# Kernel optimization log

Measured on AMD Instinct MI355X. Metric: run time of the kernel, lower is better.

Reference implementation:

```python
import jax, jax.numpy as jnp
import numpy as np

H, R, N, E, B, T = 128, 8, 10000, 50000, 2, 64
LN_EPS = 1e-5


def setup_inputs() -> dict:
    key = jax.random.key(0)
    ks = jax.random.split(key, 12)
    s = 0.05  # weight scale for numerical sanity
    return {
        "nodes": jax.random.normal(ks[0], (N, B, H), jnp.float32),
        "temporal_sequence": jax.random.normal(ks[1], (B, T, H), jnp.float32),
        "rel_W": jax.random.normal(ks[2], (R, 2 * H, H), jnp.float32) * s,
        "rel_b": jnp.zeros((R, H), jnp.float32),
        "gru_Wih": jax.random.normal(ks[3], (3 * H, H), jnp.float32) * s,
        "gru_Whh": jax.random.normal(ks[4], (3 * H, H), jnp.float32) * s,
        "gru_bih": jnp.zeros((3 * H,), jnp.float32),
        "gru_bhh": jnp.zeros((3 * H,), jnp.float32),
        "mlp_W1": jax.random.normal(ks[5], (H, 2 * H), jnp.float32) * s,
        "mlp_b1": jnp.zeros((2 * H,), jnp.float32),
        "ln_g": jnp.ones((2 * H,), jnp.float32),
        "ln_b": jnp.zeros((2 * H,), jnp.float32),
        "mlp_W2": jax.random.normal(ks[6], (2 * H, H), jnp.float32) * s,
        "mlp_b2": jnp.zeros((H,), jnp.float32),
        "src": jax.random.randint(ks[7], (E,), 0, N, jnp.int32),
        "rel": jax.random.randint(ks[8], (E,), 0, R, jnp.int32),
        "dst": jax.random.randint(ks[9], (E,), 0, N, jnp.int32),
    }


def _gru_last(x, Wih, Whh, bih, bhh):
    # x: [B, T, H] batch-first; returns last hidden state [B, H]
    xt = jnp.swapaxes(x, 0, 1)                    # [T, B, H]
    gx = xt @ Wih.T + bih                         # precompute input gates [T, B, 3H]

    def step(h, gxt):
        gh = h @ Whh.T + bhh
        xr, xz, xn = jnp.split(gxt, 3, axis=-1)
        hr, hz, hn = jnp.split(gh, 3, axis=-1)
        r = jax.nn.sigmoid(xr + hr)
        z = jax.nn.sigmoid(xz + hz)
        n = jnp.tanh(xn + r * hn)
        h = (1.0 - z) * n + z * h
        return h, None

    h0 = jnp.zeros((x.shape[0], Whh.shape[1]), x.dtype)
    hT, _ = jax.lax.scan(step, h0, gx)
    return hT


def _layernorm(x, g, b):
    mu = jnp.mean(x, axis=-1, keepdims=True)
    var = jnp.mean((x - mu) ** 2, axis=-1, keepdims=True)
    return (x - mu) * jax.lax.rsqrt(var + LN_EPS) * g + b


def reference(nodes, temporal_sequence, rel_W, rel_b, gru_Wih, gru_Whh,
              gru_bih, gru_bhh, mlp_W1, mlp_b1, ln_g, ln_b, mlp_W2, mlp_b2,
              src, rel, dst):
    # per-edge gather + concat: [E, B, 2H]
    edge_in = jnp.concatenate([nodes[src], nodes[dst]], axis=-1)
    # relation-type routed linear: loop over fixed R=8 relations, mask-select
    out = jnp.zeros((edge_in.shape[0], edge_in.shape[1], rel_W.shape[-1]), edge_in.dtype)
    for r in range(rel_W.shape[0]):
        yr = edge_in @ rel_W[r] + rel_b[r]        # [E, B, H]
        out = out + jnp.where((rel == r)[:, None, None], yr, 0.0)
    graph_state = out.mean(axis=0)                # mean over edges -> [B, H]
    graph_state = graph_state + _gru_last(temporal_sequence, gru_Wih, gru_Whh, gru_bih, gru_bhh)
    # reasoning MLP (dropout is eval-mode identity)
    h1 = graph_state @ mlp_W1 + mlp_b1            # [B, 2H]
    h1 = jax.nn.relu(_layernorm(h1, ln_g, ln_b))
    return h1 @ mlp_W2 + mlp_b2                   # [B, H]
```

## Files before the change

kernel.cpp:

```cpp
#include <hip/hip_runtime.h>
#include <hip/hip_bf16.h>
#include <math.h>

#define H 128
#define TT 64
#define TWO_H 256
#define NGX 128
#define NACC 128

typedef short short8 __attribute__((ext_vector_type(8)));
typedef __bf16 bf16x8_t __attribute__((ext_vector_type(8)));
typedef float f32x4 __attribute__((ext_vector_type(4)));
typedef unsigned int uint;

__device__ inline unsigned short bf_rne(float f) {
    __hip_bfloat16 b = __float2bfloat16(f);
    return __builtin_bit_cast(unsigned short, b);
}
__device__ inline void split_rne(float f, unsigned short& hi, unsigned short& lo) {
    __hip_bfloat16 h1 = __float2bfloat16(f);
    float fh = __bfloat162float(h1);
    hi = __builtin_bit_cast(unsigned short, h1);
    lo = bf_rne(f - fh);
}
__device__ inline f32x4 mfma_bf16(short8 a, short8 b, f32x4 c) {
    return __builtin_amdgcn_mfma_f32_16x16x32_bf16(
        __builtin_bit_cast(bf16x8_t, a), __builtin_bit_cast(bf16x8_t, b), c, 0, 0, 0);
}
__device__ inline float sigf(float x) { return 1.f / (1.f + __expf(-x)); }

__global__ void k_edges_fb(const float* __restrict__ nodes, const int* __restrict__ src,
                           const int* __restrict__ rel, const int* __restrict__ dst,
                           float* __restrict__ Sg, float* __restrict__ cntg, int E, int epb) {
    __shared__ float Sl[8 * 512];
    __shared__ float cnt[8];
    int t = threadIdx.x;
    for (int i = t; i < 8 * 512; i += 256) Sl[i] = 0.f;
    if (t < 8) cnt[t] = 0.f;
    __syncthreads();
    int e0 = blockIdx.x * epb, e1 = min(E, e0 + epb);
    int tS = ((t >> 7) << 8) + (t & 127);
    for (int e = e0; e < e1; ++e) {
        int r = rel[e];
        float vs = nodes[(size_t)src[e] * 256 + t];
        float vd = nodes[(size_t)dst[e] * 256 + t];
        Sl[r * 512 + tS] += vs;
        Sl[r * 512 + tS + 128] += vd;
        if (t == 0) cnt[r] += 1.f;
    }
    __syncthreads();
    for (int i = t; i < 8 * 512; i += 256) atomicAdd(&Sg[i], Sl[i]);
    if (t < 8) atomicAdd(&cntg[t], cnt[t]);
}

__launch_bounds__(256, 1)
__global__ void k_fused(const float* __restrict__ nodes, const int* __restrict__ src,
                        const int* __restrict__ rel, const int* __restrict__ dst,
                        const float* __restrict__ x, const float* __restrict__ Wih,
                        const float* __restrict__ bih, uint* __restrict__ csd,
                        float* __restrict__ Sg, float* __restrict__ cntg,
                        const float* __restrict__ relW, const float* __restrict__ relb,
                        float* __restrict__ gs, int* __restrict__ flags, float invE,
                        float* __restrict__ gxT2, const float* __restrict__ Whh,
                        const float* __restrict__ bhh, const float* __restrict__ W1,
                        const float* __restrict__ b1, const float* __restrict__ lng,
                        const float* __restrict__ lnb, const float* __restrict__ W2,
                        const float* __restrict__ b2v, float* __restrict__ out,
                        int N, int E, int nch, int naccum, int hist) {
    int t = threadIdx.x;
    int bid = blockIdx.x;

    if (bid >= 10 && bid < 10 + NGX) {
        int idx = bid - 10;
        __shared__ float xs[H];
        int tt = idx >> 1, bb = idx & 1;
        if (t < H) xs[t] = x[(bb * TT + tt) * H + t];
        __syncthreads();
        for (int o = t; o < 384; o += 256) {
            const float4* wp = (const float4*)(Wih + o * H);
            float acc = 0.f;
#pragma unroll
            for (int i = 0; i < 32; ++i) {
                float4 w = wp[i];
                acc += w.x * xs[4 * i] + w.y * xs[4 * i + 1] + w.z * xs[4 * i + 2] +
                       w.w * xs[4 * i + 3];
            }
            float bias = bih[o] + (o < TWO_H ? bhh[o] : 0.f);
            int g = o >> 7, j = o & 127;
            gxT2[((size_t)(bb * TT + tt) * 128 + j) * 4 + g] = acc + bias;
        }
        __syncthreads();
        if (t == 0) {
            __threadfence();
            atomicAdd(&flags[5], 1);
        }
        if (hist) {
            int per = (E + NGX - 1) / NGX;
            int e0 = idx * per, e1 = min(E, e0 + per);
            for (int e = e0 + t; e < e1; e += 256) {
                int r = rel[e];
                atomicAdd(&csd[(size_t)src[e] * 8 + r], 1u);
                atomicAdd(&csd[(size_t)dst[e] * 8 + r], 65536u);
            }
            __syncthreads();
            if (t == 0) {
                __threadfence();
                atomicAdd(&flags[2], 1);
            }
        }
        return;
    }

    if (bid >= 10 + NGX) {
        int ai = bid - 10 - NGX;
        if (t == 0) {
            while (atomicAdd(&flags[2], 0) < NGX) __builtin_amdgcn_s_sleep(8);
            __threadfence();
        }
        __syncthreads();
        int n0 = ai * nch, n1 = min(N, n0 + nch);
        float sA[8] = {0, 0, 0, 0, 0, 0, 0, 0};
        float sB[8] = {0, 0, 0, 0, 0, 0, 0, 0};
        float caR[8] = {0, 0, 0, 0, 0, 0, 0, 0};
        int n = n0;
        for (; n + 4 <= n1; n += 4) {
            float v0 = nodes[(size_t)(n + 0) * 256 + t];
            float v1 = nodes[(size_t)(n + 1) * 256 + t];
            float v2 = nodes[(size_t)(n + 2) * 256 + t];
            float v3 = nodes[(size_t)(n + 3) * 256 + t];
            uint4 a0 = *(const uint4*)(csd + (size_t)(n + 0) * 8);
            uint4 a1 = *(const uint4*)(csd + (size_t)(n + 0) * 8 + 4);
            uint4 b0 = *(const uint4*)(csd + (size_t)(n + 1) * 8);
            uint4 b1u = *(const uint4*)(csd + (size_t)(n + 1) * 8 + 4);
            uint4 c0 = *(const uint4*)(csd + (size_t)(n + 2) * 8);
            uint4 c1 = *(const uint4*)(csd + (size_t)(n + 2) * 8 + 4);
            uint4 d0 = *(const uint4*)(csd + (size_t)(n + 3) * 8);
            uint4 d1 = *(const uint4*)(csd + (size_t)(n + 3) * 8 + 4);
            uint ca[8] = {a0.x, a0.y, a0.z, a0.w, a1.x, a1.y, a1.z, a1.w};
            uint cb[8] = {b0.x, b0.y, b0.z, b0.w, b1u.x, b1u.y, b1u.z, b1u.w};
            uint cc[8] = {c0.x, c0.y, c0.z, c0.w, c1.x, c1.y, c1.z, c1.w};
            uint cd2[8] = {d0.x, d0.y, d0.z, d0.w, d1.x, d1.y, d1.z, d1.w};
#pragma unroll
            for (int r = 0; r < 8; ++r) {
                float fs0 = (float)(ca[r] & 0xffffu), fd0 = (float)(ca[r] >> 16);
                float fs1 = (float)(cb[r] & 0xffffu), fd1 = (float)(cb[r] >> 16);
                float fs2 = (float)(cc[r] & 0xffffu), fd2 = (float)(cc[r] >> 16);
                float fs3 = (float)(cd2[r] & 0xffffu), fd3 = (float)(cd2[r] >> 16);
                sA[r] += fs0 * v0 + fs1 * v1 + fs2 * v2 + fs3 * v3;
                sB[r] += fd0 * v0 + fd1 * v1 + fd2 * v2 + fd3 * v3;
                caR[r] += fs0 + fs1 + fs2 + fs3;
            }
        }
        for (; n < n1; ++n) {
            float v = nodes[(size_t)n * 256 + t];
            const uint* cp = csd + (size_t)n * 8;
            uint4 c0 = *(const uint4*)cp;
            uint4 c1 = *(const uint4*)(cp + 4);
            uint cc[8] = {c0.x, c0.y, c0.z, c0.w, c1.x, c1.y, c1.z, c1.w};
#pragma unroll
            for (int r = 0; r < 8; ++r) {
                float fs = (float)(cc[r] & 0xffffu);
                float fd = (float)(cc[r] >> 16);
                sA[r] += fs * v;
                sB[r] += fd * v;
                caR[r] += fs;
            }
        }
        int b = t >> 7, h = t & 127;
#pragma unroll
        for (int r = 0; r < 8; ++r) {
            atomicAdd(&Sg[r * 512 + b * 256 + h], sA[r]);
            atomicAdd(&Sg[r * 512 + b * 256 + 128 + h], sB[r]);
        }
        if (t == 0) {
#pragma unroll
            for (int r = 0; r < 8; ++r) atomicAdd(&cntg[r], caR[r]);
        }
        __syncthreads();
        if (t == 0) {
            __threadfence();
            atomicAdd(&flags[0], 1);
        }
        return;
    }

    if (bid >= 2) {
        int r = bid - 2;
        __shared__ float Sc[512];
        if (t == 0) {
            while (atomicAdd(&flags[0], 0) < naccum) __builtin_amdgcn_s_sleep(8);
        }
        __syncthreads();
        for (int i = t; i < 512; i += 256) Sc[i] = atomicAdd(&Sg[r * 512 + i], 0.f);
        __syncthreads();
        int b = t >> 7, h = t & 127;
        const float* Wr = relW + (size_t)r * TWO_H * H;
        float acc = 0.f;
#pragma unroll 8
        for (int c = 0; c < TWO_H; ++c) acc += Sc[b * 256 + c] * Wr[c * H + h];
        acc += atomicAdd(&cntg[r], 0.f) * relb[r * H + h];
        atomicAdd(&gs[t], acc * invE);
        __syncthreads();
        if (t == 0) {
            __threadfence();
            atomicAdd(&flags[1], 1);
        }
        return;
    }

    int b = bid;
    __shared__ __align__(16) unsigned short h2[2][3][144];
    __shared__ __align__(16) float gxs[2][8][128][4];
    __shared__ float hfl[H];
    __shared__ float gl2[H];
    __shared__ float yl[TWO_H];
    __shared__ float red[8];

    int w = t >> 6, l = t & 63;

    for (int i = t; i < 2 * 3 * 144; i += 256) ((unsigned short*)h2)[i] = 0;

    short8 Bf[6][4];
#pragma unroll
    for (int ti = 0; ti < 6; ++ti) {
        int row = ((ti >> 1) * 8 + 2 * w + (ti & 1)) * 16 + (l & 15);
#pragma unroll
        for (int kt = 0; kt < 4; ++kt) {
            const float4* wp = (const float4*)(Whh + row * H + kt * 32 + (l >> 4) * 8);
            float4 w0 = wp[0], w1 = wp[1];
            float ww[8] = {w0.x, w0.y, w0.z, w0.w, w1.x, w1.y, w1.z, w1.w};
            short8 v8;
#pragma unroll
            for (int e = 0; e < 8; ++e) v8[e] = (short)bf_rne(ww[e]);
            Bf[ti][kt] = v8;
        }
    }

    int al = l & 15;
    int rr = al < 2 ? al : 2;
    int kg = (l >> 4) * 8;

    float hpv[2] = {0.f, 0.f};
    float bhnv[2];
    int j0 = w * 32 + l;
    if (l < 16) {
        bhnv[0] = bhh[TWO_H + j0];
        bhnv[1] = bhh[TWO_H + j0 + 16];
    }

    const float* gxb = gxT2 + (size_t)b * TT * 512;

    if (t == 0) {
        while (atomicAdd(&flags[5], 0) < NGX) __builtin_amdgcn_s_sleep(2);
        __threadfence();
    }
    __syncthreads();
    {
        float* lb = &gxs[0][0][0][0];
#pragma unroll
        for (int i = 0; i < 4; ++i) {
            __builtin_amdgcn_global_load_lds(
                (const __attribute__((address_space(1))) uint*)(gxb + w * 1024 + i * 256 + l * 4),
                (__attribute__((address_space(3))) uint*)(lb + w * 1024 + i * 256),
                16, 0, 0);
        }
    }
    __syncthreads();

    __builtin_amdgcn_s_setprio(1);
    for (int c = 0; c < 8; ++c) {
        if (c < 7) {
            float* lb = &gxs[(c + 1) & 1][0][0][0];
            const float* sb = gxb + (size_t)(c + 1) * 4096;
#pragma unroll
            for (int i = 0; i < 4; ++i) {
                __builtin_amdgcn_global_load_lds(
                    (const __attribute__((address_space(1))) uint*)(sb + w * 1024 + i * 256 + l * 4),
                    (__attribute__((address_space(3))) uint*)(lb + w * 1024 + i * 256),
                    16, 0, 0);
            }
        }
#pragma unroll
        for (int i = 0; i < 8; ++i) {
            int p = i & 1, q = p ^ 1;

            short8 A[4];
#pragma unroll
            for (int kt = 0; kt < 4; ++kt)
                A[kt] = *(const short8*)&h2[p][rr][kt * 32 + kg];

            f32x4 acc[6];
#pragma unroll
            for (int ti = 0; ti < 6; ++ti) acc[ti] = (f32x4){0.f, 0.f, 0.f, 0.f};
#pragma unroll
            for (int kt = 0; kt < 4; ++kt) {
#pragma unroll
                for (int ti = 0; ti < 6; ++ti) acc[ti] = mfma_bf16(A[kt], Bf[ti][kt], acc[ti]);
            }

            if (l < 16) {
#pragma unroll
                for (int jh = 0; jh < 2; ++jh) {
                    int j = j0 + jh * 16;
                    const float4 cg = *(const float4*)&gxs[c & 1][i][j][0];
                    float ghr = acc[0 + jh][0] + acc[0 + jh][1];
                    float ghz = acc[2 + jh][0] + acc[2 + jh][1];
                    float ghn = acc[4 + jh][0] + acc[4 + jh][1];
                    float rg = sigf(cg.x + ghr);
                    float zg = sigf(cg.y + ghz);
                    float nn = cg.z + rg * (ghn + bhnv[jh]);
                    float th = 2.f * sigf(2.f * nn) - 1.f;
                    float hn2 = (1.f - zg) * th + zg * hpv[jh];
                    hpv[jh] = hn2;
                    unsigned short hh, ll;
                    split_rne(hn2, hh, ll);
                    h2[q][0][j] = hh;
                    h2[q][1][j] = ll;
                }
            }
            __builtin_amdgcn_sched_barrier(0);
            if (i == 7) {
                asm volatile("s_waitcnt vmcnt(0) lgkmcnt(0)" ::: "memory");
            } else {
                asm volatile("s_waitcnt lgkmcnt(0)" ::: "memory");
            }
            __builtin_amdgcn_s_barrier();
            __builtin_amdgcn_sched_barrier(0);
        }
    }
    __builtin_amdgcn_s_setprio(0);

    if (l < 16) {
        hfl[j0] = hpv[0];
        hfl[j0 + 16] = hpv[1];
    }
    if (t == 0) {
        while (atomicAdd(&flags[1], 0) < 8) __builtin_amdgcn_s_sleep(8);
    }
    __syncthreads();
    if (t < H) gl2[t] = atomicAdd(&gs[b * H + t], 0.f) + hfl[t];
    __syncthreads();

    float h1 = b1[t];
    for (int i = 0; i < H; ++i) h1 += gl2[i] * W1[i * TWO_H + t];
    float s1 = h1, s2 = h1 * h1;
#pragma unroll
    for (int off = 32; off; off >>= 1) {
        s1 += __shfl_xor(s1, off);
        s2 += __shfl_xor(s2, off);
    }
    if (l == 0) {
        red[w * 2] = s1;
        red[w * 2 + 1] = s2;
    }
    __syncthreads();
    {
        float S1 = red[0] + red[2] + red[4] + red[6];
        float S2 = red[1] + red[3] + red[5] + red[7];
        float mu = S1 / 256.f;
        float var = S2 / 256.f - mu * mu;
        float is = rsqrtf(var + 1e-5f);
        float y = (h1 - mu) * is * lng[t] + lnb[t];
        yl[t] = fmaxf(y, 0.f);
    }
    __syncthreads();
    if (t < H) {
        float a = b2v[t];
        for (int i = 0; i < TWO_H; ++i) a += yl[i] * W2[i * H + t];
        out[b * H + t] = a;
    }
}

extern "C" void kernel_launch(void* const* d_in, const int* in_sizes, int n_in,
                              void* d_out, int out_size, void* d_ws, size_t ws_size,
                              hipStream_t stream) {
    const float* nodes = (const float*)d_in[0];
    const float* temporal = (const float*)d_in[1];
    const float* relW = (const float*)d_in[2];
    const float* relb = (const float*)d_in[3];
    const float* gru_Wih = (const float*)d_in[4];
    const float* gru_Whh = (const float*)d_in[5];
    const float* gru_bih = (const float*)d_in[6];
    const float* gru_bhh = (const float*)d_in[7];
    const float* mlp_W1 = (const float*)d_in[8];
    const float* mlp_b1 = (const float*)d_in[9];
    const float* ln_g = (const float*)d_in[10];
    const float* ln_b = (const float*)d_in[11];
    const float* mlp_W2 = (const float*)d_in[12];
    const float* mlp_b2 = (const float*)d_in[13];
    const int* src = (const int*)d_in[14];
    const int* rel = (const int*)d_in[15];
    const int* dst = (const int*)d_in[16];
    float* out = (float*)d_out;

    int E = in_sizes[14];
    int N = in_sizes[0] / 256;

    float* ws = (float*)d_ws;
    float* gs = ws;
    float* cntg = ws + 256;
    int* flags = (int*)(ws + 264);
    float* Sg = ws + 288;
    uint* csd = (uint*)(ws + 4384);

    size_t need_hist = (size_t)(4384 + 8 * N + 65536) * 4;
    int hist = ws_size >= need_hist ? 1 : 0;

    float* gxT2 = hist ? (ws + 4384 + 8 * N) : (ws + 4384);
    size_t zbytes = hist ? (size_t)(4384 + 8 * N) * 4 : (size_t)4384 * 4;
    hipMemsetAsync(d_ws, 0, zbytes, stream);

    int naccum, nblk;
    if (hist) {
        naccum = NACC;
        nblk = 10 + NGX + NACC;
    } else {
        int epb = (E + 511) / 512;
        k_edges_fb<<<512, 256, 0, stream>>>(nodes, src, rel, dst, Sg, cntg, E, epb);
        naccum = 0;
        nblk = 10 + NGX;
    }
    int nch = (N + NACC - 1) / NACC;

    k_fused<<<nblk, 256, 0, stream>>>(nodes, src, rel, dst, temporal, gru_Wih, gru_bih,
                                      csd, Sg, cntg, relW, relb, gs, flags,
                                      1.f / (float)E, gxT2, gru_Whh, gru_bhh, mlp_W1,
                                      mlp_b1, ln_g, ln_b, mlp_W2, mlp_b2, out,
                                      N, E, nch, naccum, hist);
}
```

Baseline: 86.47 us.

## Zero histogram in-kernel, start GRU after first chunk, spread gate math across 32 lanes

The histogram buffer is now zeroed inside the GX blocks, with a completion flag, so the host memset covers only the small header. The GRU block begins prefetching once the first 16 GX blocks, which produce the first time chunk, have finished, and it waits for all GX blocks only after issuing that load. The per-step gate nonlinearity now runs on 32 lanes instead of 16 looping over two columns, using a shuffle to move the second tile's sums. This shortens the memset, the GRU startup latency and the serial per-step tail, at the cost of an extra spin-wait barrier before the histogram atomics.

```diff
diff --git a/kernel.cpp b/kernel.cpp
--- a/kernel.cpp
+++ b/kernel.cpp
@@ -72,6 +72,16 @@
 
     if (bid >= 10 && bid < 10 + NGX) {
         int idx = bid - 10;
+        if (hist) {
+            int nz = (8 * N + NGX - 1) / NGX;
+            int z0 = idx * nz, z1 = min(8 * N, z0 + nz);
+            for (int i = z0 + t; i < z1; i += 256) csd[i] = 0u;
+            __syncthreads();
+            if (t == 0) {
+                __threadfence();
+                atomicAdd(&flags[7], 1);
+            }
+        }
         __shared__ float xs[H];
         int tt = idx >> 1, bb = idx & 1;
         if (t < H) xs[t] = x[(bb * TT + tt) * H + t];
@@ -93,8 +103,14 @@
         if (t == 0) {
             __threadfence();
             atomicAdd(&flags[5], 1);
+            if (idx < 16) atomicAdd(&flags[6], 1);
         }
         if (hist) {
+            if (t == 0) {
+                while (atomicAdd(&flags[7], 0) < NGX) __builtin_amdgcn_s_sleep(2);
+                __threadfence();
+            }
+            __syncthreads();
             int per = (E + NGX - 1) / NGX;
             int e0 = idx * per, e1 = min(E, e0 + per);
             for (int e = e0 + t; e < e1; e += 256) {
@@ -240,18 +256,15 @@
     int rr = al < 2 ? al : 2;
     int kg = (l >> 4) * 8;
 
-    float hpv[2] = {0.f, 0.f};
-    float bhnv[2];
-    int j0 = w * 32 + l;
-    if (l < 16) {
-        bhnv[0] = bhh[TWO_H + j0];
-        bhnv[1] = bhh[TWO_H + j0 + 16];
-    }
+    float hp = 0.f;
+    float bhn = 0.f;
+    int jg = w * 32 + l;
+    if (l < 32) bhn = bhh[TWO_H + jg];
 
     const float* gxb = gxT2 + (size_t)b * TT * 512;
 
     if (t == 0) {
-        while (atomicAdd(&flags[5], 0) < NGX) __builtin_amdgcn_s_sleep(2);
+        while (atomicAdd(&flags[6], 0) < 16) __builtin_amdgcn_s_sleep(2);
         __threadfence();
     }
     __syncthreads();
@@ -265,6 +278,10 @@
                 16, 0, 0);
         }
     }
+    if (t == 0) {
+        while (atomicAdd(&flags[5], 0) < NGX) __builtin_amdgcn_s_sleep(2);
+        __threadfence();
+    }
     __syncthreads();
 
     __builtin_amdgcn_s_setprio(1);
@@ -298,25 +315,26 @@
                 for (int ti = 0; ti < 6; ++ti) acc[ti] = mfma_bf16(A[kt], Bf[ti][kt], acc[ti]);
             }
 
-            if (l < 16) {
-#pragma unroll
-                for (int jh = 0; jh < 2; ++jh) {
-                    int j = j0 + jh * 16;
-                    const float4 cg = *(const float4*)&gxs[c & 1][i][j][0];
-                    float ghr = acc[0 + jh][0] + acc[0 + jh][1];
-                    float ghz = acc[2 + jh][0] + acc[2 + jh][1];
-                    float ghn = acc[4 + jh][0] + acc[4 + jh][1];
-                    float rg = sigf(cg.x + ghr);
-                    float zg = sigf(cg.y + ghz);
-                    float nn = cg.z + rg * (ghn + bhnv[jh]);
-                    float th = 2.f * sigf(2.f * nn) - 1.f;
-                    float hn2 = (1.f - zg) * th + zg * hpv[jh];
-                    hpv[jh] = hn2;
-                    unsigned short hh, ll;
-                    split_rne(hn2, hh, ll);
-                    h2[q][0][j] = hh;
-                    h2[q][1][j] = ll;
-                }
+            float s0r = acc[0][0] + acc[0][1], s1r = acc[1][0] + acc[1][1];
+            float s0z = acc[2][0] + acc[2][1], s1z = acc[3][0] + acc[3][1];
+            float s0n = acc[4][0] + acc[4][1], s1n = acc[5][0] + acc[5][1];
+            float t1r = __shfl(s1r, l & 15, 32);
+            float t1z = __shfl(s1z, l & 15, 32);
+            float t1n = __shfl(s1n, l & 15, 32);
+            if (l < 32) {
+                float ghr = (l < 16) ? s0r : t1r;
+                float ghz = (l < 16) ? s0z : t1z;
+                float ghn = (l < 16) ? s0n : t1n;
+                const float4 cg = *(const float4*)&gxs[c & 1][i][jg][0];
+                float rg = sigf(cg.x + ghr);
+                float zg = sigf(cg.y + ghz);
+                float nn = cg.z + rg * (ghn + bhn);
+                float th = 2.f * sigf(2.f * nn) - 1.f;
+                hp = (1.f - zg) * th + zg * hp;
+                unsigned short hh, ll;
+                split_rne(hp, hh, ll);
+                h2[q][0][jg] = hh;
+                h2[q][1][jg] = ll;
             }
             __builtin_amdgcn_sched_barrier(0);
             if (i == 7) {
@@ -330,10 +348,7 @@
     }
     __builtin_amdgcn_s_setprio(0);
 
-    if (l < 16) {
-        hfl[j0] = hpv[0];
-        hfl[j0 + 16] = hpv[1];
-    }
+    if (l < 32) hfl[jg] = hp;
     if (t == 0) {
         while (atomicAdd(&flags[1], 0) < 8) __builtin_amdgcn_s_sleep(8);
     }
@@ -407,8 +422,7 @@
     int hist = ws_size >= need_hist ? 1 : 0;
 
     float* gxT2 = hist ? (ws + 4384 + 8 * N) : (ws + 4384);
-    size_t zbytes = hist ? (size_t)(4384 + 8 * N) * 4 : (size_t)4384 * 4;
-    hipMemsetAsync(d_ws, 0, zbytes, stream);
+    hipMemsetAsync(d_ws, 0, (size_t)4384 * 4, stream);
 
     int naccum, nblk;
     if (hist) {
```

Measured after the change: 90.23 us. 1.04x slower.

## Use 512-thread blocks to split GRU recurrence across eight waves

Applied to the files above, without the earlier changes.

The fused kernel now launches with 512 threads so the serial GRU recurrence blocks use eight waves instead of four. Each wave holds a third of the Whh fragments and computes one 16-wide slice of hidden units per gate. The K-loop is split into two independent MFMA accumulator chains to shorten the dependency chain. The other block roles are guarded to use only the first 256 threads. This is meant to cut per-step latency on the 64-step critical path, at the cost of barriers spanning more waves and idle threads in the non-GRU blocks.

```diff
diff --git a/kernel.cpp b/kernel.cpp
--- a/kernel.cpp
+++ b/kernel.cpp
@@ -53,7 +53,7 @@
     if (t < 8) atomicAdd(&cntg[t], cnt[t]);
 }
 
-__launch_bounds__(256, 1)
+__launch_bounds__(512, 1)
 __global__ void k_fused(const float* __restrict__ nodes, const int* __restrict__ src,
                         const int* __restrict__ rel, const int* __restrict__ dst,
                         const float* __restrict__ x, const float* __restrict__ Wih,
@@ -76,7 +76,7 @@
         int tt = idx >> 1, bb = idx & 1;
         if (t < H) xs[t] = x[(bb * TT + tt) * H + t];
         __syncthreads();
-        for (int o = t; o < 384; o += 256) {
+        for (int o = t; o < 384; o += 512) {
             const float4* wp = (const float4*)(Wih + o * H);
             float acc = 0.f;
 #pragma unroll
@@ -97,7 +97,7 @@
         if (hist) {
             int per = (E + NGX - 1) / NGX;
             int e0 = idx * per, e1 = min(E, e0 + per);
-            for (int e = e0 + t; e < e1; e += 256) {
+            for (int e = e0 + t; e < e1; e += 512) {
                 int r = rel[e];
                 atomicAdd(&csd[(size_t)src[e] * 8 + r], 1u);
                 atomicAdd(&csd[(size_t)dst[e] * 8 + r], 65536u);
@@ -118,63 +118,65 @@
             __threadfence();
         }
         __syncthreads();
-        int n0 = ai * nch, n1 = min(N, n0 + nch);
-        float sA[8] = {0, 0, 0, 0, 0, 0, 0, 0};
-        float sB[8] = {0, 0, 0, 0, 0, 0, 0, 0};
-        float caR[8] = {0, 0, 0, 0, 0, 0, 0, 0};
-        int n = n0;
-        for (; n + 4 <= n1; n += 4) {
-            float v0 = nodes[(size_t)(n + 0) * 256 + t];
-            float v1 = nodes[(size_t)(n + 1) * 256 + t];
-            float v2 = nodes[(size_t)(n + 2) * 256 + t];
-            float v3 = nodes[(size_t)(n + 3) * 256 + t];
-            uint4 a0 = *(const uint4*)(csd + (size_t)(n + 0) * 8);
-            uint4 a1 = *(const uint4*)(csd + (size_t)(n + 0) * 8 + 4);
-            uint4 b0 = *(const uint4*)(csd + (size_t)(n + 1) * 8);
-            uint4 b1u = *(const uint4*)(csd + (size_t)(n + 1) * 8 + 4);
-            uint4 c0 = *(const uint4*)(csd + (size_t)(n + 2) * 8);
-            uint4 c1 = *(const uint4*)(csd + (size_t)(n + 2) * 8 + 4);
-            uint4 d0 = *(const uint4*)(csd + (size_t)(n + 3) * 8);
-            uint4 d1 = *(const uint4*)(csd + (size_t)(n + 3) * 8 + 4);
-            uint ca[8] = {a0.x, a0.y, a0.z, a0.w, a1.x, a1.y, a1.z, a1.w};
-            uint cb[8] = {b0.x, b0.y, b0.z, b0.w, b1u.x, b1u.y, b1u.z, b1u.w};
-            uint cc[8] = {c0.x, c0.y, c0.z, c0.w, c1.x, c1.y, c1.z, c1.w};
-            uint cd2[8] = {d0.x, d0.y, d0.z, d0.w, d1.x, d1.y, d1.z, d1.w};
+        if (t < 256) {
+            int n0 = ai * nch, n1 = min(N, n0 + nch);
+            float sA[8] = {0, 0, 0, 0, 0, 0, 0, 0};
+            float sB[8] = {0, 0, 0, 0, 0, 0, 0, 0};
+            float caR[8] = {0, 0, 0, 0, 0, 0, 0, 0};
+            int n = n0;
+            for (; n + 4 <= n1; n += 4) {
+                float v0 = nodes[(size_t)(n + 0) * 256 + t];
+                float v1 = nodes[(size_t)(n + 1) * 256 + t];
+                float v2 = nodes[(size_t)(n + 2) * 256 + t];
+                float v3 = nodes[(size_t)(n + 3) * 256 + t];
+                uint4 a0 = *(const uint4*)(csd + (size_t)(n + 0) * 8);
+                uint4 a1 = *(const uint4*)(csd + (size_t)(n + 0) * 8 + 4);
+                uint4 b0 = *(const uint4*)(csd + (size_t)(n + 1) * 8);
+                uint4 b1u = *(const uint4*)(csd + (size_t)(n + 1) * 8 + 4);
+                uint4 c0 = *(const uint4*)(csd + (size_t)(n + 2) * 8);
+                uint4 c1 = *(const uint4*)(csd + (size_t)(n + 2) * 8 + 4);
+                uint4 d0 = *(const uint4*)(csd + (size_t)(n + 3) * 8);
+                uint4 d1 = *(const uint4*)(csd + (size_t)(n + 3) * 8 + 4);
+                uint ca[8] = {a0.x, a0.y, a0.z, a0.w, a1.x, a1.y, a1.z, a1.w};
+                uint cb[8] = {b0.x, b0.y, b0.z, b0.w, b1u.x, b1u.y, b1u.z, b1u.w};
+                uint cc[8] = {c0.x, c0.y, c0.z, c0.w, c1.x, c1.y, c1.z, c1.w};
+                uint cd2[8] = {d0.x, d0.y, d0.z, d0.w, d1.x, d1.y, d1.z, d1.w};
+#pragma unroll
+                for (int r = 0; r < 8; ++r) {
+                    float fs0 = (float)(ca[r] & 0xffffu), fd0 = (float)(ca[r] >> 16);
+                    float fs1 = (float)(cb[r] & 0xffffu), fd1 = (float)(cb[r] >> 16);
+                    float fs2 = (float)(cc[r] & 0xffffu), fd2 = (float)(cc[r] >> 16);
+                    float fs3 = (float)(cd2[r] & 0xffffu), fd3 = (float)(cd2[r] >> 16);
+                    sA[r] += fs0 * v0 + fs1 * v1 + fs2 * v2 + fs3 * v3;
+                    sB[r] += fd0 * v0 + fd1 * v1 + fd2 * v2 + fd3 * v3;
+                    caR[r] += fs0 + fs1 + fs2 + fs3;
+                }
+            }
+            for (; n < n1; ++n) {
+                float v = nodes[(size_t)n * 256 + t];
+                const uint* cp = csd + (size_t)n * 8;
+                uint4 c0 = *(const uint4*)cp;
+                uint4 c1 = *(const uint4*)(cp + 4);
+                uint cc[8] = {c0.x, c0.y, c0.z, c0.w, c1.x, c1.y, c1.z, c1.w};
+#pragma unroll
+                for (int r = 0; r < 8; ++r) {
+                    float fs = (float)(cc[r] & 0xffffu);
+                    float fd = (float)(cc[r] >> 16);
+                    sA[r] += fs * v;
+                    sB[r] += fd * v;
+                    caR[r] += fs;
+                }
+            }
+            int b = t >> 7, h = t & 127;
 #pragma unroll
             for (int r = 0; r < 8; ++r) {
-                float fs0 = (float)(ca[r] & 0xffffu), fd0 = (float)(ca[r] >> 16);
-                float fs1 = (float)(cb[r] & 0xffffu), fd1 = (float)(cb[r] >> 16);
-                float fs2 = (float)(cc[r] & 0xffffu), fd2 = (float)(cc[r] >> 16);
-                float fs3 = (float)(cd2[r] & 0xffffu), fd3 = (float)(cd2[r] >> 16);
-                sA[r] += fs0 * v0 + fs1 * v1 + fs2 * v2 + fs3 * v3;
-                sB[r] += fd0 * v0 + fd1 * v1 + fd2 * v2 + fd3 * v3;
-                caR[r] += fs0 + fs1 + fs2 + fs3;
-            }
-        }
-        for (; n < n1; ++n) {
-            float v = nodes[(size_t)n * 256 + t];
-            const uint* cp = csd + (size_t)n * 8;
-            uint4 c0 = *(const uint4*)cp;
-            uint4 c1 = *(const uint4*)(cp + 4);
-            uint cc[8] = {c0.x, c0.y, c0.z, c0.w, c1.x, c1.y, c1.z, c1.w};
-#pragma unroll
-            for (int r = 0; r < 8; ++r) {
-                float fs = (float)(cc[r] & 0xffffu);
-                float fd = (float)(cc[r] >> 16);
-                sA[r] += fs * v;
-                sB[r] += fd * v;
-                caR[r] += fs;
-            }
-        }
-        int b = t >> 7, h = t & 127;
-#pragma unroll
-        for (int r = 0; r < 8; ++r) {
-            atomicAdd(&Sg[r * 512 + b * 256 + h], sA[r]);
-            atomicAdd(&Sg[r * 512 + b * 256 + 128 + h], sB[r]);
-        }
-        if (t == 0) {
-#pragma unroll
-            for (int r = 0; r < 8; ++r) atomicAdd(&cntg[r], caR[r]);
+                atomicAdd(&Sg[r * 512 + b * 256 + h], sA[r]);
+                atomicAdd(&Sg[r * 512 + b * 256 + 128 + h], sB[r]);
+            }
+            if (t == 0) {
+#pragma unroll
+                for (int r = 0; r < 8; ++r) atomicAdd(&cntg[r], caR[r]);
+            }
         }
         __syncthreads();
         if (t == 0) {
@@ -191,15 +193,17 @@
             while (atomicAdd(&flags[0], 0) < naccum) __builtin_amdgcn_s_sleep(8);
         }
         __syncthreads();
-        for (int i = t; i < 512; i += 256) Sc[i] = atomicAdd(&Sg[r * 512 + i], 0.f);
-        __syncthreads();
-        int b = t >> 7, h = t & 127;
-        const float* Wr = relW + (size_t)r * TWO_H * H;
-        float acc = 0.f;
+        for (int i = t; i < 512; i += 512) Sc[i] = atomicAdd(&Sg[r * 512 + i], 0.f);
+        __syncthreads();
+        if (t < 256) {
+            int b = t >> 7, h = t & 127;
+            const float* Wr = relW + (size_t)r * TWO_H * H;
+            float acc = 0.f;
 #pragma unroll 8
-        for (int c = 0; c < TWO_H; ++c) acc += Sc[b * 256 + c] * Wr[c * H + h];
-        acc += atomicAdd(&cntg[r], 0.f) * relb[r * H + h];
-        atomicAdd(&gs[t], acc * invE);
+            for (int c = 0; c < TWO_H; ++c) acc += Sc[b * 256 + c] * Wr[c * H + h];
+            acc += atomicAdd(&cntg[r], 0.f) * relb[r * H + h];
+            atomicAdd(&gs[t], acc * invE);
+        }
         __syncthreads();
         if (t == 0) {
             __threadfence();
@@ -214,16 +218,16 @@
     __shared__ float hfl[H];
     __shared__ float gl2[H];
     __shared__ float yl[TWO_H];
-    __shared__ float red[8];
+    __shared__ float red[16];
 
     int w = t >> 6, l = t & 63;
 
-    for (int i = t; i < 2 * 3 * 144; i += 256) ((unsigned short*)h2)[i] = 0;
-
-    short8 Bf[6][4];
-#pragma unroll
-    for (int ti = 0; ti < 6; ++ti) {
-        int row = ((ti >> 1) * 8 + 2 * w + (ti & 1)) * 16 + (l & 15);
+    for (int i = t; i < 2 * 3 * 144; i += 512) ((unsigned short*)h2)[i] = 0;
+
+    short8 Bf[3][4];
+#pragma unroll
+    for (int g3 = 0; g3 < 3; ++g3) {
+        int row = (g3 * 8 + w) * 16 + (l & 15);
 #pragma unroll
         for (int kt = 0; kt < 4; ++kt) {
             const float4* wp = (const float4*)(Whh + row * H + kt * 32 + (l >> 4) * 8);
@@ -232,7 +236,7 @@
             short8 v8;
 #pragma unroll
             for (int e = 0; e < 8; ++e) v8[e] = (short)bf_rne(ww[e]);
-            Bf[ti][kt] = v8;
+            Bf[g3][kt] = v8;
         }
     }
 
@@ -240,13 +244,10 @@
     int rr = al < 2 ? al : 2;
     int kg = (l >> 4) * 8;
 
-    float hpv[2] = {0.f, 0.f};
-    float bhnv[2];
-    int j0 = w * 32 + l;
-    if (l < 16) {
-        bhnv[0] = bhh[TWO_H + j0];
-        bhnv[1] = bhh[TWO_H + j0 + 16];
-    }
+    float hp = 0.f;
+    float bhn = 0.f;
+    int j0 = w * 16 + l;
+    if (l < 16) bhn = bhh[TWO_H + j0];
 
     const float* gxb = gxT2 + (size_t)b * TT * 512;
 
@@ -258,10 +259,10 @@
     {
         float* lb = &gxs[0][0][0][0];
 #pragma unroll
-        for (int i = 0; i < 4; ++i) {
+        for (int i = 0; i < 2; ++i) {
             __builtin_amdgcn_global_load_lds(
-                (const __attribute__((address_space(1))) uint*)(gxb + w * 1024 + i * 256 + l * 4),
-                (__attribute__((address_space(3))) uint*)(lb + w * 1024 + i * 256),
+                (const __attribute__((address_space(1))) uint*)(gxb + w * 512 + i * 256 + l * 4),
+                (__attribute__((address_space(3))) uint*)(lb + w * 512 + i * 256),
                 16, 0, 0);
         }
     }
@@ -273,10 +274,10 @@
             float* lb = &gxs[(c + 1) & 1][0][0][0];
             const float* sb = gxb + (size_t)(c + 1) * 4096;
 #pragma unroll
-            for (int i = 0; i < 4; ++i) {
+            for (int i = 0; i < 2; ++i) {
                 __builtin_amdgcn_global_load_lds(
-                    (const __attribute__((address_space(1))) uint*)(sb + w * 1024 + i * 256 + l * 4),
-                    (__attribute__((address_space(3))) uint*)(lb + w * 1024 + i * 256),
+                    (const __attribute__((address_space(1))) uint*)(sb + w * 512 + i * 256 + l * 4),
+                    (__attribute__((address_space(3))) uint*)(lb + w * 512 + i * 256),
                     16, 0, 0);
             }
         }
@@ -289,34 +290,35 @@
             for (int kt = 0; kt < 4; ++kt)
                 A[kt] = *(const short8*)&h2[p][rr][kt * 32 + kg];
 
-            f32x4 acc[6];
-#pragma unroll
-            for (int ti = 0; ti < 6; ++ti) acc[ti] = (f32x4){0.f, 0.f, 0.f, 0.f};
-#pragma unroll
-            for (int kt = 0; kt < 4; ++kt) {
-#pragma unroll
-                for (int ti = 0; ti < 6; ++ti) acc[ti] = mfma_bf16(A[kt], Bf[ti][kt], acc[ti]);
+            f32x4 aA[3], aB[3];
+#pragma unroll
+            for (int g3 = 0; g3 < 3; ++g3) {
+                aA[g3] = (f32x4){0.f, 0.f, 0.f, 0.f};
+                aB[g3] = (f32x4){0.f, 0.f, 0.f, 0.f};
+            }
+#pragma unroll
+            for (int kt = 0; kt < 2; ++kt) {
+#pragma unroll
+                for (int g3 = 0; g3 < 3; ++g3) {
+                    aA[g3] = mfma_bf16(A[kt], Bf[g3][kt], aA[g3]);
+                    aB[g3] = mfma_bf16(A[kt + 2], Bf[g3][kt + 2], aB[g3]);
+                }
             }
 
             if (l < 16) {
-#pragma unroll
-                for (int jh = 0; jh < 2; ++jh) {
-                    int j = j0 + jh * 16;
-                    const float4 cg = *(const float4*)&gxs[c & 1][i][j][0];
-                    float ghr = acc[0 + jh][0] + acc[0 + jh][1];
-                    float ghz = acc[2 + jh][0] + acc[2 + jh][1];
-                    float ghn = acc[4 + jh][0] + acc[4 + jh][1];
-                    float rg = sigf(cg.x + ghr);
-                    float zg = sigf(cg.y + ghz);
-                    float nn = cg.z + rg * (ghn + bhnv[jh]);
-                    float th = 2.f * sigf(2.f * nn) - 1.f;
-                    float hn2 = (1.f - zg) * th + zg * hpv[jh];
-                    hpv[jh] = hn2;
-                    unsigned short hh, ll;
-                    split_rne(hn2, hh, ll);
-                    h2[q][0][j] = hh;
-                    h2[q][1][j] = ll;
-                }
+                const float4 cg = *(const float4*)&gxs[c & 1][i][j0][0];
+                float ghr = aA[0][0] + aA[0][1] + aB[0][0] + aB[0][1];
+                float ghz = aA[1][0] + aA[1][1] + aB[1][0] + aB[1][1];
+                float ghn = aA[2][0] + aA[2][1] + aB[2][0] + aB[2][1];
+                float rg = sigf(cg.x + ghr);
+                float zg = sigf(cg.y + ghz);
+                float nn = cg.z + rg * (ghn + bhn);
+                float th = 2.f * sigf(2.f * nn) - 1.f;
+                hp = (1.f - zg) * th + zg * hp;
+                unsigned short hh, ll;
+                split_rne(hp, hh, ll);
+                h2[q][0][j0] = hh;
+                h2[q][1][j0] = ll;
             }
             __builtin_amdgcn_sched_barrier(0);
             if (i == 7) {
@@ -330,10 +332,7 @@
     }
     __builtin_amdgcn_s_setprio(0);
 
-    if (l < 16) {
-        hfl[j0] = hpv[0];
-        hfl[j0 + 16] = hpv[1];
-    }
+    if (l < 16) hfl[j0] = hp;
     if (t == 0) {
         while (atomicAdd(&flags[1], 0) < 8) __builtin_amdgcn_s_sleep(8);
     }
@@ -341,9 +340,13 @@
     if (t < H) gl2[t] = atomicAdd(&gs[b * H + t], 0.f) + hfl[t];
     __syncthreads();
 
-    float h1 = b1[t];
-    for (int i = 0; i < H; ++i) h1 += gl2[i] * W1[i * TWO_H + t];
-    float s1 = h1, s2 = h1 * h1;
+    float h1 = 0.f;
+    if (t < 256) {
+        h1 = b1[t];
+        for (int i = 0; i < H; ++i) h1 += gl2[i] * W1[i * TWO_H + t];
+    }
+    float s1 = (t < 256) ? h1 : 0.f;
+    float s2 = (t < 256) ? h1 * h1 : 0.f;
 #pragma unroll
     for (int off = 32; off; off >>= 1) {
         s1 += __shfl_xor(s1, off);
@@ -355,13 +358,15 @@
     }
     __syncthreads();
     {
-        float S1 = red[0] + red[2] + red[4] + red[6];
-        float S2 = red[1] + red[3] + red[5] + red[7];
+        float S1 = red[0] + red[2] + red[4] + red[6] + red[8] + red[10] + red[12] + red[14];
+        float S2 = red[1] + red[3] + red[5] + red[7] + red[9] + red[11] + red[13] + red[15];
         float mu = S1 / 256.f;
         float var = S2 / 256.f - mu * mu;
         float is = rsqrtf(var + 1e-5f);
-        float y = (h1 - mu) * is * lng[t] + lnb[t];
-        yl[t] = fmaxf(y, 0.f);
+        if (t < 256) {
+            float y = (h1 - mu) * is * lng[t] + lnb[t];
+            yl[t] = fmaxf(y, 0.f);
+        }
     }
     __syncthreads();
     if (t < H) {
@@ -422,7 +427,7 @@
     }
     int nch = (N + NACC - 1) / NACC;
 
-    k_fused<<<nblk, 256, 0, stream>>>(nodes, src, rel, dst, temporal, gru_Wih, gru_bih,
+    k_fused<<<nblk, 512, 0, stream>>>(nodes, src, rel, dst, temporal, gru_Wih, gru_bih,
                                       csd, Sg, cntg, relW, relb, gs, flags,
                                       1.f / (float)E, gxT2, gru_Whh, gru_bhh, mlp_W1,
                                       mlp_b1, ln_g, ln_b, mlp_W2, mlp_b2, out,
```

Result: no change. 86.09 us (median of 2 runs) (-0.4%).
